# Performance work log

Hardware: AMD Instinct MI355X
Metric: run time of the kernel (lower is better)

## Reference

```python
import jax, jax.numpy as jnp
import numpy as np

S = 8192        # seq_length
H2 = 1024       # 2 * lstm_hidden_size
A = 2048        # attention_hidden_size
E = 768         # embedding_dim == pos_embedding_dim


def _bahdanau_weights(sentence, length, ctx, W_s, b_s, W_c, b_c, v, b_v):
    # sentence: [1, S, H2], ctx: [1, E_ctx]
    u = jnp.einsum('bsh,ha->bsa', sentence, W_s) + b_s \
        + (ctx @ W_c + b_c)[:, None, :]                    # [1, S, A]
    e = jnp.einsum('bsa,a->bs', jnp.tanh(u), v) + b_v       # [1, S]
    mask = jnp.arange(S)[None, :] >= length[:, None]        # [1, S] key mask
    e = jnp.where(mask, -jnp.inf, e)
    all_inf = jnp.all(mask, axis=1)                         # [1]
    # guard fully-masked rows so softmax stays finite, then zero them (matches torch)
    e_safe = jnp.where(all_inf[:, None], jnp.zeros_like(e), e)
    w = jax.nn.softmax(e_safe, axis=1)
    return jnp.where(all_inf[:, None], 0.0, w)              # [1, S]


def setup_inputs() -> dict:
    key = jax.random.key(0)
    ks = jax.random.split(key, 24)
    f = jax.random.normal
    sc_s = 1.0 / np.sqrt(H2)
    sc_c = 1.0 / np.sqrt(E)
    sc_v = 1.0 / np.sqrt(A)
    inp = {
        'sentence': f(ks[0], (1, S, H2), jnp.float32),
        'length': jax.random.randint(ks[1], (1,), 0, S),
        'pos_embedding': f(ks[2], (1, E), jnp.float32),
        'cardinal_phrase_embedding': f(ks[3], (1, E), jnp.float32),
        'headline_embedding': f(ks[4], (1, E), jnp.float32),
    }
    i = 5
    for tag in ('p', 'c', 'h'):
        inp[f'W_sent_{tag}'] = f(ks[i], (H2, A), jnp.float32) * sc_s; i += 1
        inp[f'b_sent_{tag}'] = f(ks[i], (A,), jnp.float32) * sc_s; i += 1
        inp[f'W_ctx_{tag}'] = f(ks[i], (E, A), jnp.float32) * sc_c; i += 1
        inp[f'b_ctx_{tag}'] = f(ks[i], (A,), jnp.float32) * sc_c; i += 1
        inp[f'v_{tag}'] = f(ks[i], (A,), jnp.float32) * sc_v; i += 1
        inp[f'bv_{tag}'] = f(ks[i], (), jnp.float32) * sc_v; i += 1
    return inp


def reference(sentence, length, pos_embedding, cardinal_phrase_embedding,
              headline_embedding,
              W_sent_p, b_sent_p, W_ctx_p, b_ctx_p, v_p, bv_p,
              W_sent_c, b_sent_c, W_ctx_c, b_ctx_c, v_c, bv_c,
              W_sent_h, b_sent_h, W_ctx_h, b_ctx_h, v_h, bv_h):
    w_pos = _bahdanau_weights(sentence, length, pos_embedding,
                              W_sent_p, b_sent_p, W_ctx_p, b_ctx_p, v_p, bv_p)
    w_card = _bahdanau_weights(sentence, length, cardinal_phrase_embedding,
                               W_sent_c, b_sent_c, W_ctx_c, b_ctx_c, v_c, bv_c)
    w_head = _bahdanau_weights(sentence, length, headline_embedding,
                               W_sent_h, b_sent_h, W_ctx_h, b_ctx_h, v_h, bv_h)
    fused = (w_pos + w_card + w_head) / 3.0                 # [1, S]
    return jnp.einsum('bs,bsh->bh', fused, sentence)        # [1, H2]
```

## Files before the change

kernel.cpp:

```cpp
#include <hip/hip_runtime.h>
#include <hip/hip_bf16.h>
#include <stdint.h>


namespace {

constexpr int S = 8192;
constexpr int H = 1024;
constexpr int A = 2048;
constexpr int E = 768;

typedef __bf16 bf16x8 __attribute__((ext_vector_type(8)));
typedef float f32x4 __attribute__((ext_vector_type(4)));

__device__ __forceinline__ void gl_lds16(const void* g, void* l) {
  __builtin_amdgcn_global_load_lds(
      (const __attribute__((address_space(1))) void*)g,
      (__attribute__((address_space(3))) void*)l, 16, 0, 0);
}

__global__ __launch_bounds__(256)
void k_prep(const float* __restrict__ sentence, __bf16* __restrict__ sentB,
            const float* __restrict__ Wp, const float* __restrict__ Wc_s,
            const float* __restrict__ Wh, __bf16* __restrict__ WtB,
            const float* __restrict__ ctx_p, const float* __restrict__ ctx_c,
            const float* __restrict__ ctx_h,
            const float* __restrict__ Wcx_p, const float* __restrict__ Wcx_c,
            const float* __restrict__ Wcx_h,
            const float* __restrict__ bs_p, const float* __restrict__ bs_c,
            const float* __restrict__ bs_h,
            const float* __restrict__ bc_p, const float* __restrict__ bc_c,
            const float* __restrict__ bc_h,
            float* __restrict__ ctxb_q, float* __restrict__ e_arr,
            const int* __restrict__ length, float* __restrict__ out, int n_out) {
  __shared__ float tile[64][65];
  int b = blockIdx.x;
  int t = threadIdx.x;

  if (b < 4096) {
    int len = min(max(length[0], 0), S);
    int lenp = (len + 63) & ~63;
    if (b * 2 >= lenp) return;
    int g = b * 256 + t;
    const float4* s4 = (const float4*)sentence + (size_t)g * 2;
    float4 a = s4[0], c = s4[1];
    bf16x8 o;
    o[0] = (__bf16)a.x; o[1] = (__bf16)a.y; o[2] = (__bf16)a.z; o[3] = (__bf16)a.w;
    o[4] = (__bf16)c.x; o[5] = (__bf16)c.y; o[6] = (__bf16)c.z; o[7] = (__bf16)c.w;
    *((bf16x8*)sentB + g) = o;
  } else if (b < 5632) {
    int r = b - 4096;
    int head = r >> 9; r &= 511;
    const float* W = head == 0 ? Wp : (head == 1 ? Wc_s : Wh);
    __bf16* dst = WtB + (size_t)head * A * H;
    int a0 = (r & 31) * 64;
    int k0 = (r >> 5) * 64;
#pragma unroll
    for (int i = 0; i < 16; ++i) {
      int idx = t + i * 256;
      int rr = idx >> 6, cc = idx & 63;
      tile[cc][rr] = W[(size_t)(k0 + rr) * A + a0 + cc];
    }
    __syncthreads();
#pragma unroll
    for (int i = 0; i < 16; ++i) {
      int idx = t + i * 256;
      int al = idx >> 6, kl = idx & 63;
      dst[(size_t)(a0 + al) * H + k0 + kl] = (__bf16)tile[al][kl];
    }
  } else if (b < 5728) {
    int r = b - 5632;
    int head = r >> 5;
    int sub = r & 31;
    int ablk = sub & 7;
    int eq = sub >> 3;
    const float* ctx = head == 0 ? ctx_p : (head == 1 ? ctx_c : ctx_h);
    const float* Wc  = head == 0 ? Wcx_p : (head == 1 ? Wcx_c : Wcx_h);
    int a = ablk * 256 + t;
    float s = 0.f;
    if (eq == 0) {
      const float* bs = head == 0 ? bs_p : (head == 1 ? bs_c : bs_h);
      const float* bc = head == 0 ? bc_p : (head == 1 ? bc_c : bc_h);
      s = bs[a] + bc[a];
    }
    int e0 = eq * 192;
#pragma unroll 8
    for (int e = e0; e < e0 + 192; ++e) s = fmaf(ctx[e], Wc[(size_t)e * A + a], s);
    ctxb_q[eq * 3 * A + head * A + a] = s;
  } else {
    int idx = (b - 5728) * 256 + t;
    float4 z = {0.f, 0.f, 0.f, 0.f};
    int total = 6144 + (n_out >> 2);
    for (int i = idx; i < total; i += 2048) {
      if (i < 6144) ((float4*)e_arr)[i] = z;
      else ((float4*)out)[i - 6144] = z;
    }
  }
}

__global__ __launch_bounds__(256)
void k_gemm_e(const __bf16* __restrict__ sentB, const __bf16* __restrict__ WtB,
              const float* __restrict__ ctxb_q,
              const float* __restrict__ v_p, const float* __restrict__ v_c,
              const float* __restrict__ v_h,
              const int* __restrict__ length, float* __restrict__ e_out) {
  int m0 = blockIdx.x * 64;
  int len = min(max(length[0], 0), S);
  if (m0 >= len) return;
  int n0 = blockIdx.y * 64;
  int head = blockIdx.z;
  const float* v  = head == 0 ? v_p : (head == 1 ? v_c : v_h);
  const __bf16* Wt = WtB + (size_t)head * A * H;
  float* e_h = e_out + head * S;

  __shared__ __align__(16) __bf16 lsA[4 * 2048];
  __shared__ __align__(16) __bf16 lsB[4 * 2048];
  __shared__ float e_part[64];

  int tid = threadIdx.x;
  if (tid < 64) e_part[tid] = 0.f;

  int lane = tid & 63;
  int wave = tid >> 6;
  int wm = wave >> 1, wn = wave & 1;
  int quad = lane >> 4, l16 = lane & 15;

  f32x4 acc[2][2];
#pragma unroll
  for (int i = 0; i < 2; ++i)
#pragma unroll
    for (int j = 0; j < 2; ++j) acc[i][j] = (f32x4){0.f, 0.f, 0.f, 0.f};

  const __bf16* gA0 = sentB + (size_t)(m0 + (tid >> 2)) * H + ((tid & 3) * 8);
  const __bf16* gB0 = Wt + (size_t)(n0 + (tid >> 2)) * H + ((tid & 3) * 8);

#define STAGE(bufi, kk)                                           \
  do {                                                            \
    gl_lds16(gA0 + (kk), lsA + (bufi) * 2048 + tid * 8);          \
    gl_lds16(gB0 + (kk), lsB + (bufi) * 2048 + tid * 8);          \
  } while (0)

#define COMPUTE(bufi)                                                                          \
  do {                                                                                         \
    bf16x8 af[2], bfv[2];                                                                      \
    _Pragma("unroll")                                                                          \
    for (int i = 0; i < 2; ++i)                                                                \
      af[i] = *(const bf16x8*)&lsA[(bufi) * 2048 + (wm * 32 + i * 16 + l16) * 32 + quad * 8];  \
    _Pragma("unroll")                                                                          \
    for (int j = 0; j < 2; ++j)                                                                \
      bfv[j] = *(const bf16x8*)&lsB[(bufi) * 2048 + (wn * 32 + j * 16 + l16) * 32 + quad * 8]; \
    _Pragma("unroll")                                                                          \
    for (int i = 0; i < 2; ++i)                                                                \
      _Pragma("unroll")                                                                        \
      for (int j = 0; j < 2; ++j)                                                              \
        acc[i][j] = __builtin_amdgcn_mfma_f32_16x16x32_bf16(af[i], bfv[j], acc[i][j], 0, 0, 0);\
  } while (0)

  STAGE(0, 0);
  STAGE(1, 32);
  STAGE(2, 64);
#pragma unroll 1
  for (int t = 0; t < 29; ++t) {
    asm volatile("s_waitcnt vmcnt(4)");
    __builtin_amdgcn_s_barrier();
    __builtin_amdgcn_sched_barrier(0);
    STAGE((t + 3) & 3, (t + 3) * 32);
    COMPUTE(t & 3);
  }
  asm volatile("s_waitcnt vmcnt(4)");
  __builtin_amdgcn_s_barrier();
  __builtin_amdgcn_sched_barrier(0);
  COMPUTE(1);
  asm volatile("s_waitcnt vmcnt(2)");
  __builtin_amdgcn_s_barrier();
  __builtin_amdgcn_sched_barrier(0);
  COMPUTE(2);
  asm volatile("s_waitcnt vmcnt(0)");
  __builtin_amdgcn_s_barrier();
  __builtin_amdgcn_sched_barrier(0);
  COMPUTE(3);

#undef STAGE
#undef COMPUTE

  float vj[2], cbj[2];
#pragma unroll
  for (int j = 0; j < 2; ++j) {
    int col = n0 + wn * 32 + j * 16 + l16;
    vj[j] = v[col];
    cbj[j] = ctxb_q[head * A + col] + ctxb_q[3 * A + head * A + col] +
             ctxb_q[6 * A + head * A + col] + ctxb_q[9 * A + head * A + col];
  }
#pragma unroll
  for (int i = 0; i < 2; ++i) {
#pragma unroll
    for (int r = 0; r < 4; ++r) {
      float p = 0.f;
#pragma unroll
      for (int j = 0; j < 2; ++j) {
        float u = acc[i][j][r] + cbj[j];
        float ex = __expf(2.f * u);
        float th = 1.f - 2.f / (ex + 1.f);
        p = fmaf(th, vj[j], p);
      }
      p += __shfl_xor(p, 1);
      p += __shfl_xor(p, 2);
      p += __shfl_xor(p, 4);
      p += __shfl_xor(p, 8);
      if (l16 == 0) atomicAdd(&e_part[wm * 32 + i * 16 + quad * 4 + r], p);
    }
  }
  __syncthreads();
  if (tid < 64) atomicAdd(&e_h[m0 + tid], e_part[tid]);
}

__global__ void k_out(const float* __restrict__ sent, const float* __restrict__ e_arr,
                      const int* __restrict__ length, float* __restrict__ out) {
  int len = min(max(length[0], 0), S);
  int r0 = blockIdx.x * 16;
  if (r0 >= len) return;
  int tid = threadIdx.x;

  __shared__ float red[3][4];
  __shared__ float sstat[6];
  __shared__ float wrow[16];

#pragma unroll
  for (int h = 0; h < 3; ++h) {
    const float* e_h = e_arr + h * S;
    float m = -3.4e38f;
    for (int s = tid; s < len; s += 256) m = fmaxf(m, e_h[s]);
#pragma unroll
    for (int o = 32; o >= 1; o >>= 1) m = fmaxf(m, __shfl_xor(m, o));
    if ((tid & 63) == 0) red[h][tid >> 6] = m;
  }
  __syncthreads();
  if (tid < 3) sstat[tid * 2] = fmaxf(fmaxf(red[tid][0], red[tid][1]),
                                      fmaxf(red[tid][2], red[tid][3]));
  __syncthreads();
#pragma unroll
  for (int h = 0; h < 3; ++h) {
    const float* e_h = e_arr + h * S;
    float mm = sstat[h * 2];
    float ss = 0.f;
    for (int s = tid; s < len; s += 256) ss += __expf(e_h[s] - mm);
#pragma unroll
    for (int o = 32; o >= 1; o >>= 1) ss += __shfl_xor(ss, o);
    if ((tid & 63) == 0) red[h][tid >> 6] = ss;
  }
  __syncthreads();
  if (tid < 3) sstat[tid * 2 + 1] = red[tid][0] + red[tid][1] + red[tid][2] + red[tid][3];
  __syncthreads();

  if (tid < 16 && r0 + tid < len) {
    int r = r0 + tid;
    wrow[tid] = (__expf(e_arr[r] - sstat[0]) / sstat[1] +
                 __expf(e_arr[S + r] - sstat[2]) / sstat[3] +
                 __expf(e_arr[2 * S + r] - sstat[4]) / sstat[5]) * (1.f / 3.f);
  }
  __syncthreads();

  int col = tid * 4;
  int rend = min(r0 + 16, len);
  float4 acc = {0.f, 0.f, 0.f, 0.f};
  for (int r = r0; r < rend; ++r) {
    float w = wrow[r - r0];
    float4 x = *(const float4*)(sent + (size_t)r * H + col);
    acc.x = fmaf(w, x.x, acc.x);
    acc.y = fmaf(w, x.y, acc.y);
    acc.z = fmaf(w, x.z, acc.z);
    acc.w = fmaf(w, x.w, acc.w);
  }
  atomicAdd(&out[col + 0], acc.x);
  atomicAdd(&out[col + 1], acc.y);
  atomicAdd(&out[col + 2], acc.z);
  atomicAdd(&out[col + 3], acc.w);
}

}

extern "C" void kernel_launch(void* const* d_in, const int* in_sizes, int n_in,
                              void* d_out, int out_size, void* d_ws, size_t ws_size,
                              hipStream_t stream) {
  const float* sentence = (const float*)d_in[0];
  const int* length     = (const int*)d_in[1];
  const float* ctx_p = (const float*)d_in[2];
  const float* ctx_c = (const float*)d_in[3];
  const float* ctx_h = (const float*)d_in[4];
  const float* W_s[3] = {(const float*)d_in[5],  (const float*)d_in[11], (const float*)d_in[17]};
  const float* b_s[3] = {(const float*)d_in[6],  (const float*)d_in[12], (const float*)d_in[18]};
  const float* W_c[3] = {(const float*)d_in[7],  (const float*)d_in[13], (const float*)d_in[19]};
  const float* b_c[3] = {(const float*)d_in[8],  (const float*)d_in[14], (const float*)d_in[20]};
  const float* v_[3]  = {(const float*)d_in[9],  (const float*)d_in[15], (const float*)d_in[21]};
  float* out = (float*)d_out;

  char* ws = (char*)d_ws;
  __bf16* sentB  = (__bf16*)(ws);
  __bf16* WtB    = (__bf16*)(ws + 16777216);
  float* ctxb_q  = (float*)(ws + 29360128);
  float* e_arr   = (float*)(ws + 29458432);

  k_prep<<<5736, 256, 0, stream>>>(sentence, sentB,
                                   W_s[0], W_s[1], W_s[2], WtB,
                                   ctx_p, ctx_c, ctx_h,
                                   W_c[0], W_c[1], W_c[2],
                                   b_s[0], b_s[1], b_s[2],
                                   b_c[0], b_c[1], b_c[2], ctxb_q, e_arr,
                                   length, out, out_size);
  k_gemm_e<<<dim3(S / 64, A / 64, 3), 256, 0, stream>>>(sentB, WtB, ctxb_q,
                                                        v_[0], v_[1], v_[2], length, e_arr);
  k_out<<<S / 16, 256, 0, stream>>>(sentence, e_arr, length, out);
}
```

Baseline: 230.3 us.

## Widen GEMM tile to 64x128 with XCD-aware panel mapping and split softmax stats

```diff
diff --git a/kernel.cpp b/kernel.cpp
--- a/kernel.cpp
+++ b/kernel.cpp
@@ -56,17 +56,24 @@
     int a0 = (r & 31) * 64;
     int k0 = (r >> 5) * 64;
 #pragma unroll
-    for (int i = 0; i < 16; ++i) {
+    for (int i = 0; i < 8; ++i) {
       int idx = t + i * 256;
-      int rr = idx >> 6, cc = idx & 63;
-      tile[cc][rr] = W[(size_t)(k0 + rr) * A + a0 + cc];
+      int rr = idx >> 5;
+      int cc = (idx & 31) * 2;
+      float2 w2 = *(const float2*)&W[(size_t)(k0 + rr) * A + a0 + cc];
+      tile[cc][rr] = w2.x;
+      tile[cc + 1][rr] = w2.y;
     }
     __syncthreads();
 #pragma unroll
-    for (int i = 0; i < 16; ++i) {
+    for (int i = 0; i < 8; ++i) {
       int idx = t + i * 256;
-      int al = idx >> 6, kl = idx & 63;
-      dst[(size_t)(a0 + al) * H + k0 + kl] = (__bf16)tile[al][kl];
+      int al = idx >> 5;
+      int kl = (idx & 31) * 2;
+      union { ushort2 u; __bf16 h[2]; } o;
+      o.h[0] = (__bf16)tile[al][kl];
+      o.h[1] = (__bf16)tile[al][kl + 1];
+      *(ushort2*)&dst[(size_t)(a0 + al) * H + k0 + kl] = o.u;
     }
   } else if (b < 5728) {
     int r = b - 5632;
@@ -104,17 +111,24 @@
               const float* __restrict__ v_p, const float* __restrict__ v_c,
               const float* __restrict__ v_h,
               const int* __restrict__ length, float* __restrict__ e_out) {
-  int m0 = blockIdx.x * 64;
+  int bid = blockIdx.x;
+  int xcd = bid & 7;
+  int j = bid >> 3;
+  int mt = j / 6;
+  int pl = j - mt * 6;
+  int panel = xcd * 6 + pl;
+  int n0 = (panel & 15) * 128;
+  int head = panel >> 4;
+
+  int m0 = mt * 64;
   int len = min(max(length[0], 0), S);
   if (m0 >= len) return;
-  int n0 = blockIdx.y * 64;
-  int head = blockIdx.z;
   const float* v  = head == 0 ? v_p : (head == 1 ? v_c : v_h);
   const __bf16* Wt = WtB + (size_t)head * A * H;
   float* e_h = e_out + head * S;
 
-  __shared__ __align__(16) __bf16 lsA[4 * 2048];
-  __shared__ __align__(16) __bf16 lsB[4 * 2048];
+  __shared__ __align__(16) __bf16 lsA[3 * 2048];
+  __shared__ __align__(16) __bf16 lsB[3 * 4096];
   __shared__ float e_part[64];
 
   int tid = threadIdx.x;
@@ -125,71 +139,67 @@
   int wm = wave >> 1, wn = wave & 1;
   int quad = lane >> 4, l16 = lane & 15;
 
-  f32x4 acc[2][2];
+  f32x4 acc[2][4];
 #pragma unroll
   for (int i = 0; i < 2; ++i)
 #pragma unroll
-    for (int j = 0; j < 2; ++j) acc[i][j] = (f32x4){0.f, 0.f, 0.f, 0.f};
+    for (int j2 = 0; j2 < 4; ++j2) acc[i][j2] = (f32x4){0.f, 0.f, 0.f, 0.f};
 
   const __bf16* gA0 = sentB + (size_t)(m0 + (tid >> 2)) * H + ((tid & 3) * 8);
   const __bf16* gB0 = Wt + (size_t)(n0 + (tid >> 2)) * H + ((tid & 3) * 8);
+  const __bf16* gB1 = gB0 + (size_t)64 * H;
 
 #define STAGE(bufi, kk)                                           \
   do {                                                            \
     gl_lds16(gA0 + (kk), lsA + (bufi) * 2048 + tid * 8);          \
-    gl_lds16(gB0 + (kk), lsB + (bufi) * 2048 + tid * 8);          \
+    gl_lds16(gB0 + (kk), lsB + (bufi) * 4096 + tid * 8);          \
+    gl_lds16(gB1 + (kk), lsB + (bufi) * 4096 + 2048 + tid * 8);   \
   } while (0)
 
 #define COMPUTE(bufi)                                                                          \
   do {                                                                                         \
-    bf16x8 af[2], bfv[2];                                                                      \
+    bf16x8 af[2], bfv[4];                                                                      \
     _Pragma("unroll")                                                                          \
     for (int i = 0; i < 2; ++i)                                                                \
       af[i] = *(const bf16x8*)&lsA[(bufi) * 2048 + (wm * 32 + i * 16 + l16) * 32 + quad * 8];  \
     _Pragma("unroll")                                                                          \
-    for (int j = 0; j < 2; ++j)                                                                \
-      bfv[j] = *(const bf16x8*)&lsB[(bufi) * 2048 + (wn * 32 + j * 16 + l16) * 32 + quad * 8]; \
+    for (int jj = 0; jj < 4; ++jj)                                                             \
+      bfv[jj] = *(const bf16x8*)&lsB[(bufi) * 4096 + (wn * 64 + jj * 16 + l16) * 32 + quad * 8]; \
     _Pragma("unroll")                                                                          \
     for (int i = 0; i < 2; ++i)                                                                \
       _Pragma("unroll")                                                                        \
-      for (int j = 0; j < 2; ++j)                                                              \
-        acc[i][j] = __builtin_amdgcn_mfma_f32_16x16x32_bf16(af[i], bfv[j], acc[i][j], 0, 0, 0);\
+      for (int jj = 0; jj < 4; ++jj)                                                           \
+        acc[i][jj] = __builtin_amdgcn_mfma_f32_16x16x32_bf16(af[i], bfv[jj], acc[i][jj], 0, 0, 0);\
   } while (0)
 
   STAGE(0, 0);
   STAGE(1, 32);
-  STAGE(2, 64);
+  int cur = 0, pf = 2;
 #pragma unroll 1
-  for (int t = 0; t < 29; ++t) {
-    asm volatile("s_waitcnt vmcnt(4)");
+  for (int t = 0; t < 31; ++t) {
+    asm volatile("s_waitcnt vmcnt(3)");
     __builtin_amdgcn_s_barrier();
     __builtin_amdgcn_sched_barrier(0);
-    STAGE((t + 3) & 3, (t + 3) * 32);
-    COMPUTE(t & 3);
-  }
-  asm volatile("s_waitcnt vmcnt(4)");
-  __builtin_amdgcn_s_barrier();
-  __builtin_amdgcn_sched_barrier(0);
-  COMPUTE(1);
-  asm volatile("s_waitcnt vmcnt(2)");
-  __builtin_amdgcn_s_barrier();
-  __builtin_amdgcn_sched_barrier(0);
-  COMPUTE(2);
+    if (t < 30) STAGE(pf, (t + 2) * 32);
+    COMPUTE(cur);
+    cur = cur == 2 ? 0 : cur + 1;
+    pf = pf == 2 ? 0 : pf + 1;
+  }
   asm volatile("s_waitcnt vmcnt(0)");
   __builtin_amdgcn_s_barrier();
   __builtin_amdgcn_sched_barrier(0);
-  COMPUTE(3);
+  COMPUTE(cur);
 
 #undef STAGE
 #undef COMPUTE
 
-  float vj[2], cbj[2];
-#pragma unroll
-  for (int j = 0; j < 2; ++j) {
-    int col = n0 + wn * 32 + j * 16 + l16;
-    vj[j] = v[col];
-    cbj[j] = ctxb_q[head * A + col] + ctxb_q[3 * A + head * A + col] +
-             ctxb_q[6 * A + head * A + col] + ctxb_q[9 * A + head * A + col];
+  float vj[4], cbj[4];
+#pragma unroll
+  for (int j2 = 0; j2 < 4; ++j2) {
+    int col = n0 + wn * 64 + j2 * 16 + l16;
+    vj[j2] = v[col];
+    cbj[j2] = ctxb_q[head * A + col] + ctxb_q[3 * A + head * A + col] +
+              ctxb_q[6 * A + head * A + col] + ctxb_q[9 * A + head * A + col];
   }
 #pragma unroll
   for (int i = 0; i < 2; ++i) {
@@ -197,11 +207,11 @@
     for (int r = 0; r < 4; ++r) {
       float p = 0.f;
 #pragma unroll
-      for (int j = 0; j < 2; ++j) {
-        float u = acc[i][j][r] + cbj[j];
+      for (int j2 = 0; j2 < 4; ++j2) {
+        float u = acc[i][j2][r] + cbj[j2];
         float ex = __expf(2.f * u);
         float th = 1.f - 2.f / (ex + 1.f);
-        p = fmaf(th, vj[j], p);
+        p = fmaf(th, vj[j2], p);
       }
       p += __shfl_xor(p, 1);
       p += __shfl_xor(p, 2);
@@ -214,49 +224,52 @@
   if (tid < 64) atomicAdd(&e_h[m0 + tid], e_part[tid]);
 }
 
+__global__ void k_stats(const float* __restrict__ e_arr, const int* __restrict__ length,
+                        float* __restrict__ stats) {
+  int head = blockIdx.x;
+  const float* e_h = e_arr + head * S;
+  int len = min(max(length[0], 0), S);
+  int tid = threadIdx.x;
+  __shared__ float red[4];
+  __shared__ float bmax;
+
+  float m = -3.4e38f;
+  for (int s = tid; s < len; s += 256) m = fmaxf(m, e_h[s]);
+#pragma unroll
+  for (int o = 32; o >= 1; o >>= 1) m = fmaxf(m, __shfl_xor(m, o));
+  if ((tid & 63) == 0) red[tid >> 6] = m;
+  __syncthreads();
+  if (tid == 0) bmax = fmaxf(fmaxf(red[0], red[1]), fmaxf(red[2], red[3]));
+  __syncthreads();
+  float mm = bmax;
+
+  float ss = 0.f;
+  for (int s = tid; s < len; s += 256) ss += __expf(e_h[s] - mm);
+#pragma unroll
+  for (int o = 32; o >= 1; o >>= 1) ss += __shfl_xor(ss, o);
+  __syncthreads();
+  if ((tid & 63) == 0) red[tid >> 6] = ss;
+  __syncthreads();
+  if (tid == 0) {
+    stats[head * 2 + 0] = mm;
+    stats[head * 2 + 1] = red[0] + red[1] + red[2] + red[3];
+  }
+}
+
 __global__ void k_out(const float* __restrict__ sent, const float* __restrict__ e_arr,
-                      const int* __restrict__ length, float* __restrict__ out) {
+                      const float* __restrict__ stats, const int* __restrict__ length,
+                      float* __restrict__ out) {
   int len = min(max(length[0], 0), S);
   int r0 = blockIdx.x * 16;
   if (r0 >= len) return;
   int tid = threadIdx.x;
 
-  __shared__ float red[3][4];
-  __shared__ float sstat[6];
   __shared__ float wrow[16];
-
-#pragma unroll
-  for (int h = 0; h < 3; ++h) {
-    const float* e_h = e_arr + h * S;
-    float m = -3.4e38f;
-    for (int s = tid; s < len; s += 256) m = fmaxf(m, e_h[s]);
-#pragma unroll
-    for (int o = 32; o >= 1; o >>= 1) m = fmaxf(m, __shfl_xor(m, o));
-    if ((tid & 63) == 0) red[h][tid >> 6] = m;
-  }
-  __syncthreads();
-  if (tid < 3) sstat[tid * 2] = fmaxf(fmaxf(red[tid][0], red[tid][1]),
-                                      fmaxf(red[tid][2], red[tid][3]));
-  __syncthreads();
-#pragma unroll
-  for (int h = 0; h < 3; ++h) {
-    const float* e_h = e_arr + h * S;
-    float mm = sstat[h * 2];
-    float ss = 0.f;
-    for (int s = tid; s < len; s += 256) ss += __expf(e_h[s] - mm);
-#pragma unroll
-    for (int o = 32; o >= 1; o >>= 1) ss += __shfl_xor(ss, o);
-    if ((tid & 63) == 0) red[h][tid >> 6] = ss;
-  }
-  __syncthreads();
-  if (tid < 3) sstat[tid * 2 + 1] = red[tid][0] + red[tid][1] + red[tid][2] + red[tid][3];
-  __syncthreads();
-
   if (tid < 16 && r0 + tid < len) {
     int r = r0 + tid;
-    wrow[tid] = (__expf(e_arr[r] - sstat[0]) / sstat[1] +
-                 __expf(e_arr[S + r] - sstat[2]) / sstat[3] +
-                 __expf(e_arr[2 * S + r] - sstat[4]) / sstat[5]) * (1.f / 3.f);
+    wrow[tid] = (__expf(e_arr[r] - stats[0]) / stats[1] +
+                 __expf(e_arr[S + r] - stats[2]) / stats[3] +
+                 __expf(e_arr[2 * S + r] - stats[4]) / stats[5]) * (1.f / 3.f);
   }
   __syncthreads();
 
@@ -299,6 +312,7 @@
   __bf16* WtB    = (__bf16*)(ws + 16777216);
   float* ctxb_q  = (float*)(ws + 29360128);
   float* e_arr   = (float*)(ws + 29458432);
+  float* stats   = (float*)(ws + 29556736);
 
   k_prep<<<5736, 256, 0, stream>>>(sentence, sentB,
                                    W_s[0], W_s[1], W_s[2], WtB,
@@ -307,7 +321,8 @@
                                    b_s[0], b_s[1], b_s[2],
                                    b_c[0], b_c[1], b_c[2], ctxb_q, e_arr,
                                    length, out, out_size);
-  k_gemm_e<<<dim3(S / 64, A / 64, 3), 256, 0, stream>>>(sentB, WtB, ctxb_q,
-                                                        v_[0], v_[1], v_[2], length, e_arr);
-  k_out<<<S / 16, 256, 0, stream>>>(sentence, e_arr, length, out);
-}
+  k_gemm_e<<<6144, 256, 0, stream>>>(sentB, WtB, ctxb_q,
+                                     v_[0], v_[1], v_[2], length, e_arr);
+  k_stats<<<3, 256, 0, stream>>>(e_arr, length, stats);
+  k_out<<<S / 16, 256, 0, stream>>>(sentence, e_arr, stats, length, out);
+}
```

Result: faster. 213.5 us (-7.3%).
